# Performance work log

Measured on AMD Instinct MI355X. Metric: run time of the kernel, lower is better.

The kernel has to match this reference:

```python
import jax, jax.numpy as jnp
import numpy as np

HID = 256
N, D, K, EPOCHS = 100000, 512, 5, 2


def _lin(x, w, b):
    return x @ w.T + b


def setup_inputs() -> dict:
    key = jax.random.key(0)
    ks = jax.random.split(key, 16)
    s = 0.05
    return {
        "x0": jax.random.normal(ks[0], (N, D), jnp.float32),
        "x1": jax.random.normal(ks[1], (N, D), jnp.float32),
        "Hin0_w": jax.random.normal(ks[2], (HID, D), jnp.float32) * s,
        "Hin0_b": jax.random.normal(ks[3], (HID,), jnp.float32) * s,
        "Hin1_w": jax.random.normal(ks[4], (HID, D), jnp.float32) * s,
        "Hin1_b": jax.random.normal(ks[5], (HID,), jnp.float32) * s,
        "w0_w": jax.random.normal(ks[6], (HID, HID), jnp.float32) * s,
        "w0_b": jax.random.normal(ks[7], (HID,), jnp.float32) * s,
        "w1_w": jax.random.normal(ks[8], (HID, HID), jnp.float32) * s,
        "w1_b": jax.random.normal(ks[9], (HID,), jnp.float32) * s,
        "w2_w": jax.random.normal(ks[10], (HID, HID), jnp.float32) * s,
        "w2_b": jax.random.normal(ks[11], (HID,), jnp.float32) * s,
        "edge0": jax.random.randint(ks[12], (2, N * K), 0, N, dtype=jnp.int32),
        "edge1": jax.random.randint(ks[13], (2, N * K), 0, N, dtype=jnp.int32),
        "k": K,
        "update_epoch": EPOCHS,
    }


def reference(x0, x1, Hin0_w, Hin0_b, Hin1_w, Hin1_b, w0_w, w0_b,
              w1_w, w1_b, w2_w, w2_b, edge0, edge1, k, update_epoch):
    xs = (x0, x1)
    edges = (edge0, edge1)
    Hws = ((Hin0_w, Hin0_b), (Hin1_w, Hin1_b))
    n_views = len(xs)

    # per-view input projections: h_init[v] = H_ins[v](train_view[v])
    h_inits = [_lin(x, w, b) for x, (w, b) in zip(xs, Hws)]

    finals = []
    for v in range(n_views):
        # neighbor table: node i's k neighbors are edge[1][i*k : (i+1)*k]
        nbr_idx = edges[v][1].reshape(-1, k)  # [N, k]
        # cross-view self term: mean over other views of w2(h_init_other)
        slf = _lin(h_inits[1 - v], w2_w, w2_b)  # [N, HID] (nv-1 == 1)
        h = h_inits[v]
        for _ in range(update_epoch):
            h = _lin(h, w0_w, w0_b)
            # mean_j w1(h[nbr_j]) == w1(mean_j h[nbr_j]) since w1 is affine
            nbr_mean = h[nbr_idx].mean(axis=1)  # [N, HID] gather + reduce
            h = h + _lin(nbr_mean, w1_w, w1_b) + slf
        finals.append(jax.nn.relu(h))

    # average final embeddings across views
    h_out = sum(finals) / n_views
    return h_out
```

## Files before the change

kernel.cpp:

```cpp
#include <hip/hip_runtime.h>

#define NN 100000
#define DD 512
#define HH 256
#define KNB 5

typedef __attribute__((ext_vector_type(8))) short short8v;
typedef __attribute__((ext_vector_type(4))) short short4v;
typedef __attribute__((ext_vector_type(4))) float float4v;

static __device__ __forceinline__ float bf2f(unsigned short u) {
  union { unsigned int i; float f; } c;
  c.i = ((unsigned int)u) << 16;
  return c.f;
}
static __device__ __forceinline__ unsigned short f2bf(float f) {
  union { float f; unsigned int i; } c;
  c.f = f;
  unsigned int u = c.i;
  u += 0x7FFFu + ((u >> 16) & 1u);
  return (unsigned short)(u >> 16);
}

#define GLOAD16(g, l) __builtin_amdgcn_global_load_lds( \
    (const __attribute__((address_space(1))) unsigned int*)(g), \
    (__attribute__((address_space(3))) unsigned int*)(l), 16, 0, 0)

__global__ void cvt2(const float* __restrict__ s0, short* __restrict__ d0,
                     const float* __restrict__ s1, short* __restrict__ d1) {
  const int S1 = (HH * DD) / 4;
  int i = blockIdx.x * blockDim.x + threadIdx.x;
  if (i >= 2 * S1) return;
  const float* s = (i < S1) ? s0 : s1;
  short* d = (i < S1) ? d0 : d1;
  int j = (i < S1) ? i : i - S1;
  float4 v = reinterpret_cast<const float4*>(s)[j];
  short4v o;
  o[0] = (short)f2bf(v.x); o[1] = (short)f2bf(v.y);
  o[2] = (short)f2bf(v.z); o[3] = (short)f2bf(v.w);
  reinterpret_cast<short4v*>(d)[j] = o;
}

__global__ void prep_w01(const float* __restrict__ w0, const float* __restrict__ w1,
                         const float* __restrict__ w2, const float* __restrict__ b0,
                         const float* __restrict__ b1, const float* __restrict__ b2,
                         short* __restrict__ Bcat, float* __restrict__ bc) {
  int i = blockIdx.x;
  int j = threadIdx.x;
  Bcat[(size_t)i * 768 + j]       = (short)f2bf(w0[i * 256 + j]);
  Bcat[(size_t)i * 768 + 512 + j] = (short)f2bf(w2[i * 256 + j]);
  float acc = 0.f;
  for (int k = 0; k < 256; ++k)
    acc = fmaf(w1[i * 256 + k], w0[k * 256 + j], acc);
  Bcat[(size_t)i * 768 + 256 + j] = (short)f2bf(acc);
  if (j == 0) {
    float s = b0[i] + b1[i] + b2[i];
    for (int k = 0; k < 256; ++k) s = fmaf(w1[i * 256 + k], b0[k], s);
    bc[i] = s;
  }
}

__global__ __launch_bounds__(512) void proj_k(
    const float* __restrict__ Af0, const float* __restrict__ Af1,
    const short* __restrict__ Bw0, const short* __restrict__ Bw1,
    const float* __restrict__ bi0, const float* __restrict__ bi1,
    short* __restrict__ Cb0, short* __restrict__ Cb1)
{
  const float* Af = blockIdx.y ? Af1 : Af0;
  const short* Bw = blockIdx.y ? Bw1 : Bw0;
  const float* bias = blockIdx.y ? bi1 : bi0;
  short* Cb = blockIdx.y ? Cb1 : Cb0;

  __shared__ __align__(16) char BsRaw[256 * 64 * 2];
  __shared__ __align__(16) char AsRaw[128 * 64 * 4];

  const int tid = threadIdx.x;
  const int lane = tid & 63;
  const int wave = tid >> 6;
  const int wr = wave >> 2;
  const int wc = wave & 3;
  const int row0 = blockIdx.x * 128;

  float4v acc[4][4];
#pragma unroll
  for (int m = 0; m < 4; ++m)
#pragma unroll
    for (int n = 0; n < 4; ++n) acc[m][n] = (float4v)0.f;

  for (int k0 = 0; k0 < DD; k0 += 64) {
#pragma unroll
    for (int q = 0; q < 4; ++q) {
      int ch = q * 512 + tid;
      int r = ch >> 3, pc = ch & 7;
      int lc = pc ^ (r & 7);
      GLOAD16(Bw + (size_t)r * DD + k0 + lc * 8, BsRaw + (q * 512 + wave * 64) * 16);
    }
#pragma unroll
    for (int q = 0; q < 4; ++q) {
      int ch = q * 512 + tid;
      int r = ch >> 4, pc = ch & 15;
      int lc = pc ^ (r & 15);
      int rg = min(row0 + r, NN - 1);
      GLOAD16(Af + (size_t)rg * DD + k0 + lc * 4, AsRaw + (q * 512 + wave * 64) * 16);
    }
    __syncthreads();

#pragma unroll
    for (int kk = 0; kk < 2; ++kk) {
      const int ckb = kk * 4 + (lane >> 4);
      short8v a[4], b[4];
#pragma unroll
      for (int n = 0; n < 4; ++n) {
        int rb = wc * 64 + n * 16 + (lane & 15);
        b[n] = *reinterpret_cast<const short8v*>(BsRaw + rb * 128 + ((ckb ^ (rb & 7)) << 4));
      }
#pragma unroll
      for (int m = 0; m < 4; ++m) {
        int ra = wr * 64 + m * 16 + (lane & 15);
        int ck0 = kk * 8 + (lane >> 4) * 2;
        float4v f0 = *reinterpret_cast<const float4v*>(AsRaw + ra * 256 + ((ck0 ^ (ra & 15)) << 4));
        float4v f1 = *reinterpret_cast<const float4v*>(AsRaw + ra * 256 + (((ck0 + 1) ^ (ra & 15)) << 4));
        short8v av;
        av[0] = (short)f2bf(f0[0]); av[1] = (short)f2bf(f0[1]);
        av[2] = (short)f2bf(f0[2]); av[3] = (short)f2bf(f0[3]);
        av[4] = (short)f2bf(f1[0]); av[5] = (short)f2bf(f1[1]);
        av[6] = (short)f2bf(f1[2]); av[7] = (short)f2bf(f1[3]);
        a[m] = av;
      }
#pragma unroll
      for (int m = 0; m < 4; ++m)
#pragma unroll
        for (int n = 0; n < 4; ++n)
          acc[m][n] = __builtin_amdgcn_mfma_f32_16x16x32_bf16(b[n], a[m], acc[m][n], 0, 0, 0);
    }
    __syncthreads();
  }

  const int crow = lane & 15;
  const int cg = (lane >> 4) * 4;
#pragma unroll
  for (int m = 0; m < 4; ++m) {
    int rg = row0 + wr * 64 + m * 16 + crow;
    if (rg >= NN) continue;
#pragma unroll
    for (int n = 0; n < 4; ++n) {
      int colb = wc * 64 + n * 16 + cg;
      size_t off = (size_t)rg * HH + colb;
      float4v bi = *reinterpret_cast<const float4v*>(bias + colb);
      short4v o;
#pragma unroll
      for (int i = 0; i < 4; ++i) o[i] = (short)f2bf(acc[m][n][i] + bi[i]);
      *reinterpret_cast<short4v*>(Cb + off) = o;
    }
  }
}

template<int EPI>
__global__ __launch_bounds__(512) void epoch2(
    const short* __restrict__ D0_, const short* __restrict__ C0_,
    short* __restrict__ O0_, const int* __restrict__ n0_,
    const short* __restrict__ D1_, const short* __restrict__ C1_,
    short* __restrict__ O1_, const int* __restrict__ n1_,
    const short* __restrict__ Bw, const float* __restrict__ bias,
    float* __restrict__ Of, const short* __restrict__ Fin)
{
  __shared__ __align__(16) char BsRaw[2 * 16384];
  __shared__ __align__(16) char AsRaw[2 * 8192];
  __shared__ int nbrL[128][KNB];

  const short* D  = blockIdx.y ? D1_ : D0_;
  const short* Cc = blockIdx.y ? C1_ : C0_;
  short* Ob       = blockIdx.y ? O1_ : O0_;
  const int* nbr  = blockIdx.y ? n1_ : n0_;

  const int tid = threadIdx.x;
  const int lane = tid & 63;
  const int wave = tid >> 6;
  const int wr = wave >> 2;
  const int wc = wave & 3;
  const int row0 = blockIdx.x * 128;

  for (int e = tid; e < 128 * KNB; e += 512) {
    int r = e / KNB;
    int rg = min(row0 + r, NN - 1);
    nbrL[r][e - r * KNB] = nbr[rg * KNB + (e - r * KNB)];
  }

  {
#pragma unroll
    for (int q = 0; q < 2; ++q) {
      int ch = q * 512 + tid;
      int r = ch >> 2, pc = ch & 3;
      int lc = pc ^ ((r >> 1) & 3);
      GLOAD16(Bw + (size_t)r * 768 + lc * 8, BsRaw + (q * 512 + wave * 64) * 16);
    }
    int r = tid >> 2, pc = tid & 3;
    int lc = pc ^ ((r >> 1) & 3);
    int rg = min(row0 + r, NN - 1);
    GLOAD16(D + (size_t)rg * HH + lc * 8, AsRaw + (wave * 64) * 16);
  }
  __syncthreads();

  float4v acc[4][4];
#pragma unroll
  for (int m = 0; m < 4; ++m)
#pragma unroll
    for (int n = 0; n < 4; ++n) acc[m][n] = (float4v)0.f;

  for (int s = 0; s < 24; ++s) {
    const int sn = s + 1;
    if (sn < 24) {
      char* Bn = BsRaw + (sn & 1) * 16384;
#pragma unroll
      for (int q = 0; q < 2; ++q) {
        int ch = q * 512 + tid;
        int r = ch >> 2, pc = ch & 3;
        int lc = pc ^ ((r >> 1) & 3);
        GLOAD16(Bw + (size_t)r * 768 + sn * 32 + lc * 8, Bn + (q * 512 + wave * 64) * 16);
      }
      char* An = AsRaw + (sn & 1) * 8192;
      int r = tid >> 2, pc = tid & 3;
      int lc = pc ^ ((r >> 1) & 3);
      if (sn < 8 || sn >= 16) {
        const short* Ps = (sn < 8) ? (D + sn * 32) : (Cc + (sn * 32 - 512));
        int rg = min(row0 + r, NN - 1);
        GLOAD16(Ps + (size_t)rg * HH + lc * 8, An + (wave * 64) * 16);
      } else {
        const int kb = sn * 32 - 256;
        const short* Dk = D + kb + lc * 8;
        float a8[8] = {0.f, 0.f, 0.f, 0.f, 0.f, 0.f, 0.f, 0.f};
#pragma unroll
        for (int j = 0; j < KNB; ++j) {
          short8v v = *reinterpret_cast<const short8v*>(Dk + (size_t)nbrL[r][j] * HH);
#pragma unroll
          for (int x = 0; x < 8; ++x) a8[x] += bf2f((unsigned short)v[x]);
        }
        short8v o;
#pragma unroll
        for (int x = 0; x < 8; ++x) o[x] = (short)f2bf(a8[x] * 0.2f);
        *reinterpret_cast<short8v*>(An + tid * 16) = o;
      }
    }
    {
      const char* Bc = BsRaw + (s & 1) * 16384;
      const char* Ac = AsRaw + (s & 1) * 8192;
      const int ckb = lane >> 4;
      short8v a[4], b[4];
#pragma unroll
      for (int n = 0; n < 4; ++n) {
        int rb = wc * 64 + n * 16 + (lane & 15);
        b[n] = *reinterpret_cast<const short8v*>(Bc + rb * 64 + ((ckb ^ ((rb >> 1) & 3)) << 4));
      }
#pragma unroll
      for (int m = 0; m < 4; ++m) {
        int ra = wr * 64 + m * 16 + (lane & 15);
        a[m] = *reinterpret_cast<const short8v*>(Ac + ra * 64 + ((ckb ^ ((ra >> 1) & 3)) << 4));
      }
#pragma unroll
      for (int m = 0; m < 4; ++m)
#pragma unroll
        for (int n = 0; n < 4; ++n)
          acc[m][n] = __builtin_amdgcn_mfma_f32_16x16x32_bf16(b[n], a[m], acc[m][n], 0, 0, 0);
    }
    __syncthreads();
  }

  const int crow = lane & 15;
  const int cg = (lane >> 4) * 4;
#pragma unroll
  for (int m = 0; m < 4; ++m) {
    int rg = row0 + wr * 64 + m * 16 + crow;
    if (rg >= NN) continue;
#pragma unroll
    for (int n = 0; n < 4; ++n) {
      int colb = wc * 64 + n * 16 + cg;
      size_t off = (size_t)rg * HH + colb;
      float4v bi = *reinterpret_cast<const float4v*>(bias + colb);
      float v[4];
#pragma unroll
      for (int i = 0; i < 4; ++i) v[i] = acc[m][n][i] + bi[i];
      if constexpr (EPI >= 2) {
#pragma unroll
        for (int i = 0; i < 4; ++i) v[i] = fmaxf(v[i], 0.f);
      }
      if constexpr (EPI <= 2) {
        short4v o;
#pragma unroll
        for (int i = 0; i < 4; ++i) o[i] = (short)f2bf(v[i]);
        *reinterpret_cast<short4v*>(Ob + off) = o;
      } else {
        short4v f4 = *reinterpret_cast<const short4v*>(Fin + off);
        float4v o;
#pragma unroll
        for (int i = 0; i < 4; ++i)
          o[i] = (v[i] + bf2f((unsigned short)f4[i])) * 0.5f;
        *reinterpret_cast<float4v*>(Of + off) = o;
      }
    }
  }
}

extern "C" void kernel_launch(void* const* d_in, const int* in_sizes, int n_in,
                              void* d_out, int out_size, void* d_ws, size_t ws_size,
                              hipStream_t stream) {
  const float* x0  = (const float*)d_in[0];
  const float* x1  = (const float*)d_in[1];
  const float* wh0 = (const float*)d_in[2];
  const float* bh0 = (const float*)d_in[3];
  const float* wh1 = (const float*)d_in[4];
  const float* bh1 = (const float*)d_in[5];
  const float* w0  = (const float*)d_in[6];
  const float* b0  = (const float*)d_in[7];
  const float* w1  = (const float*)d_in[8];
  const float* b1  = (const float*)d_in[9];
  const float* w2  = (const float*)d_in[10];
  const float* b2  = (const float*)d_in[11];
  const int* e0    = (const int*)d_in[12];
  const int* e1    = (const int*)d_in[13];
  const int* nbr0  = e0 + (size_t)NN * KNB;
  const int* nbr1  = e1 + (size_t)NN * KNB;
  float* out       = (float*)d_out;

  char* ws = (char*)d_ws;
  size_t off = 0;
  auto alloc = [&](size_t bytes) -> void* {
    off = (off + 255) & ~(size_t)255;
    void* p = ws + off;
    off += bytes;
    return p;
  };

  short* Wh0  = (short*)alloc((size_t)HH * DD * 2);
  short* Wh1  = (short*)alloc((size_t)HH * DD * 2);
  short* Bcat = (short*)alloc((size_t)HH * 768 * 2);
  float* bc   = (float*)alloc((size_t)HH * 4);
  const size_t NB = (size_t)NN * HH * 2;
  short* hi0 = (short*)alloc(NB);
  short* hi1 = (short*)alloc(NB);
  short* hb0 = (short*)alloc(NB);
  short* hb1 = (short*)alloc(NB);
  short* f0  = (short*)alloc(NB);

  cvt2<<<dim3(256), dim3(256), 0, stream>>>(wh0, Wh0, wh1, Wh1);
  prep_w01<<<dim3(256), dim3(256), 0, stream>>>(w0, w1, w2, b0, b1, b2, Bcat, bc);

  proj_k<<<dim3((NN + 127) / 128, 2), dim3(512), 0, stream>>>(
      x0, x1, Wh0, Wh1, bh0, bh1, hi0, hi1);

  dim3 ge((NN + 127) / 128);

  epoch2<0><<<dim3(ge.x, 2), dim3(512), 0, stream>>>(
      hi0, hi1, hb0, nbr0,  hi1, hi0, hb1, nbr1,  Bcat, bc, nullptr, nullptr);

  epoch2<2><<<dim3(ge.x, 1), dim3(512), 0, stream>>>(
      hb0, hi1, f0, nbr0,   hb0, hi1, f0, nbr0,   Bcat, bc, nullptr, nullptr);

  epoch2<3><<<dim3(ge.x, 1), dim3(512), 0, stream>>>(
      hb1, hi0, nullptr, nbr1,  hb1, hi0, nullptr, nbr1,  Bcat, bc, out, f0);

  (void)in_sizes; (void)n_in; (void)out_size; (void)ws_size;
}
```

Baseline: 630.1 us.

## Shrink projection tile, restructure epoch kernel to single-buffered K64 steps, split launches

The projection kernel now uses 64-row tiles with half the accumulators and A staging, and its launch bounds request more resident blocks. The epoch kernel drops the double-buffered K32 software pipeline for a single-buffered K64 loop with a sync after each load stage. The fused two-view launch is split into separate per-view launches. The aim is higher occupancy and less register and LDS pressure, with other resident blocks hiding latency. The cost is losing the explicit load/compute overlap inside each block and paying extra launches.

```diff
diff --git a/kernel.cpp b/kernel.cpp
--- a/kernel.cpp
+++ b/kernel.cpp
@@ -60,7 +60,7 @@
   }
 }
 
-__global__ __launch_bounds__(512) void proj_k(
+__global__ __launch_bounds__(512, 6) void proj_k(
     const float* __restrict__ Af0, const float* __restrict__ Af1,
     const short* __restrict__ Bw0, const short* __restrict__ Bw1,
     const float* __restrict__ bi0, const float* __restrict__ bi1,
@@ -72,18 +72,18 @@
   short* Cb = blockIdx.y ? Cb1 : Cb0;
 
   __shared__ __align__(16) char BsRaw[256 * 64 * 2];
-  __shared__ __align__(16) char AsRaw[128 * 64 * 4];
+  __shared__ __align__(16) char AsRaw[64 * 64 * 4];
 
   const int tid = threadIdx.x;
   const int lane = tid & 63;
   const int wave = tid >> 6;
   const int wr = wave >> 2;
   const int wc = wave & 3;
-  const int row0 = blockIdx.x * 128;
-
-  float4v acc[4][4];
-#pragma unroll
-  for (int m = 0; m < 4; ++m)
+  const int row0 = blockIdx.x * 64;
+
+  float4v acc[2][4];
+#pragma unroll
+  for (int m = 0; m < 2; ++m)
 #pragma unroll
     for (int n = 0; n < 4; ++n) acc[m][n] = (float4v)0.f;
 
@@ -96,7 +96,7 @@
       GLOAD16(Bw + (size_t)r * DD + k0 + lc * 8, BsRaw + (q * 512 + wave * 64) * 16);
     }
 #pragma unroll
-    for (int q = 0; q < 4; ++q) {
+    for (int q = 0; q < 2; ++q) {
       int ch = q * 512 + tid;
       int r = ch >> 4, pc = ch & 15;
       int lc = pc ^ (r & 15);
@@ -108,15 +108,15 @@
 #pragma unroll
     for (int kk = 0; kk < 2; ++kk) {
       const int ckb = kk * 4 + (lane >> 4);
-      short8v a[4], b[4];
+      short8v a[2], b[4];
 #pragma unroll
       for (int n = 0; n < 4; ++n) {
         int rb = wc * 64 + n * 16 + (lane & 15);
         b[n] = *reinterpret_cast<const short8v*>(BsRaw + rb * 128 + ((ckb ^ (rb & 7)) << 4));
       }
 #pragma unroll
-      for (int m = 0; m < 4; ++m) {
-        int ra = wr * 64 + m * 16 + (lane & 15);
+      for (int m = 0; m < 2; ++m) {
+        int ra = wr * 32 + m * 16 + (lane & 15);
         int ck0 = kk * 8 + (lane >> 4) * 2;
         float4v f0 = *reinterpret_cast<const float4v*>(AsRaw + ra * 256 + ((ck0 ^ (ra & 15)) << 4));
         float4v f1 = *reinterpret_cast<const float4v*>(AsRaw + ra * 256 + (((ck0 + 1) ^ (ra & 15)) << 4));
@@ -128,7 +128,7 @@
         a[m] = av;
       }
 #pragma unroll
-      for (int m = 0; m < 4; ++m)
+      for (int m = 0; m < 2; ++m)
 #pragma unroll
         for (int n = 0; n < 4; ++n)
           acc[m][n] = __builtin_amdgcn_mfma_f32_16x16x32_bf16(b[n], a[m], acc[m][n], 0, 0, 0);
@@ -139,8 +139,8 @@
   const int crow = lane & 15;
   const int cg = (lane >> 4) * 4;
 #pragma unroll
-  for (int m = 0; m < 4; ++m) {
-    int rg = row0 + wr * 64 + m * 16 + crow;
+  for (int m = 0; m < 2; ++m) {
+    int rg = row0 + wr * 32 + m * 16 + crow;
     if (rg >= NN) continue;
 #pragma unroll
     for (int n = 0; n < 4; ++n) {
@@ -156,22 +156,15 @@
 }
 
 template<int EPI>
-__global__ __launch_bounds__(512) void epoch2(
-    const short* __restrict__ D0_, const short* __restrict__ C0_,
-    short* __restrict__ O0_, const int* __restrict__ n0_,
-    const short* __restrict__ D1_, const short* __restrict__ C1_,
-    short* __restrict__ O1_, const int* __restrict__ n1_,
+__global__ __launch_bounds__(512, 4) void epoch_k(
+    const short* __restrict__ D, const short* __restrict__ Cc,
     const short* __restrict__ Bw, const float* __restrict__ bias,
-    float* __restrict__ Of, const short* __restrict__ Fin)
+    short* __restrict__ Ob, float* __restrict__ Of,
+    const short* __restrict__ Fin, const int* __restrict__ nbr)
 {
-  __shared__ __align__(16) char BsRaw[2 * 16384];
-  __shared__ __align__(16) char AsRaw[2 * 8192];
+  __shared__ __align__(16) char BsRaw[256 * 64 * 2];
+  __shared__ __align__(16) char AsRaw[128 * 64 * 2];
   __shared__ int nbrL[128][KNB];
-
-  const short* D  = blockIdx.y ? D1_ : D0_;
-  const short* Cc = blockIdx.y ? C1_ : C0_;
-  short* Ob       = blockIdx.y ? O1_ : O0_;
-  const int* nbr  = blockIdx.y ? n1_ : n0_;
 
   const int tid = threadIdx.x;
   const int lane = tid & 63;
@@ -186,75 +179,66 @@
     nbrL[r][e - r * KNB] = nbr[rg * KNB + (e - r * KNB)];
   }
 
-  {
-#pragma unroll
-    for (int q = 0; q < 2; ++q) {
+  float4v acc[4][4];
+#pragma unroll
+  for (int m = 0; m < 4; ++m)
+#pragma unroll
+    for (int n = 0; n < 4; ++n) acc[m][n] = (float4v)0.f;
+
+  for (int k0 = 0; k0 < 768; k0 += 64) {
+#pragma unroll
+    for (int q = 0; q < 4; ++q) {
       int ch = q * 512 + tid;
-      int r = ch >> 2, pc = ch & 3;
-      int lc = pc ^ ((r >> 1) & 3);
-      GLOAD16(Bw + (size_t)r * 768 + lc * 8, BsRaw + (q * 512 + wave * 64) * 16);
-    }
-    int r = tid >> 2, pc = tid & 3;
-    int lc = pc ^ ((r >> 1) & 3);
-    int rg = min(row0 + r, NN - 1);
-    GLOAD16(D + (size_t)rg * HH + lc * 8, AsRaw + (wave * 64) * 16);
-  }
-  __syncthreads();
-
-  float4v acc[4][4];
-#pragma unroll
-  for (int m = 0; m < 4; ++m)
-#pragma unroll
-    for (int n = 0; n < 4; ++n) acc[m][n] = (float4v)0.f;
-
-  for (int s = 0; s < 24; ++s) {
-    const int sn = s + 1;
-    if (sn < 24) {
-      char* Bn = BsRaw + (sn & 1) * 16384;
+      int r = ch >> 3, pc = ch & 7;
+      int lc = pc ^ (r & 7);
+      GLOAD16(Bw + (size_t)r * 768 + k0 + lc * 8, BsRaw + (q * 512 + wave * 64) * 16);
+    }
+    if (k0 < 256 || k0 >= 512) {
+      const short* H = (k0 < 256) ? (D + k0) : (Cc + (k0 - 512));
 #pragma unroll
       for (int q = 0; q < 2; ++q) {
         int ch = q * 512 + tid;
-        int r = ch >> 2, pc = ch & 3;
-        int lc = pc ^ ((r >> 1) & 3);
-        GLOAD16(Bw + (size_t)r * 768 + sn * 32 + lc * 8, Bn + (q * 512 + wave * 64) * 16);
-      }
-      char* An = AsRaw + (sn & 1) * 8192;
-      int r = tid >> 2, pc = tid & 3;
-      int lc = pc ^ ((r >> 1) & 3);
-      if (sn < 8 || sn >= 16) {
-        const short* Ps = (sn < 8) ? (D + sn * 32) : (Cc + (sn * 32 - 512));
+        int r = ch >> 3, pc = ch & 7;
+        int lc = pc ^ (r & 7);
         int rg = min(row0 + r, NN - 1);
-        GLOAD16(Ps + (size_t)rg * HH + lc * 8, An + (wave * 64) * 16);
-      } else {
-        const int kb = sn * 32 - 256;
-        const short* Dk = D + kb + lc * 8;
+        GLOAD16(H + (size_t)rg * HH + lc * 8, AsRaw + (q * 512 + wave * 64) * 16);
+      }
+    } else {
+      const int kb = k0 - 256;
+#pragma unroll
+      for (int q = 0; q < 2; ++q) {
+        int ch = q * 512 + tid;
+        int r = ch >> 3, pc = ch & 7;
+        int lc = pc ^ (r & 7);
         float a8[8] = {0.f, 0.f, 0.f, 0.f, 0.f, 0.f, 0.f, 0.f};
 #pragma unroll
         for (int j = 0; j < KNB; ++j) {
-          short8v v = *reinterpret_cast<const short8v*>(Dk + (size_t)nbrL[r][j] * HH);
+          int id = nbrL[r][j];
+          short8v v = *reinterpret_cast<const short8v*>(D + (size_t)id * HH + kb + lc * 8);
 #pragma unroll
           for (int x = 0; x < 8; ++x) a8[x] += bf2f((unsigned short)v[x]);
         }
         short8v o;
 #pragma unroll
         for (int x = 0; x < 8; ++x) o[x] = (short)f2bf(a8[x] * 0.2f);
-        *reinterpret_cast<short8v*>(An + tid * 16) = o;
-      }
-    }
-    {
-      const char* Bc = BsRaw + (s & 1) * 16384;
-      const char* Ac = AsRaw + (s & 1) * 8192;
-      const int ckb = lane >> 4;
+        *reinterpret_cast<short8v*>(AsRaw + ch * 16) = o;
+      }
+    }
+    __syncthreads();
+
+#pragma unroll
+    for (int kk = 0; kk < 2; ++kk) {
+      const int ckb = kk * 4 + (lane >> 4);
       short8v a[4], b[4];
 #pragma unroll
       for (int n = 0; n < 4; ++n) {
         int rb = wc * 64 + n * 16 + (lane & 15);
-        b[n] = *reinterpret_cast<const short8v*>(Bc + rb * 64 + ((ckb ^ ((rb >> 1) & 3)) << 4));
+        b[n] = *reinterpret_cast<const short8v*>(BsRaw + rb * 128 + ((ckb ^ (rb & 7)) << 4));
       }
 #pragma unroll
       for (int m = 0; m < 4; ++m) {
         int ra = wr * 64 + m * 16 + (lane & 15);
-        a[m] = *reinterpret_cast<const short8v*>(Ac + ra * 64 + ((ckb ^ ((ra >> 1) & 3)) << 4));
+        a[m] = *reinterpret_cast<const short8v*>(AsRaw + ra * 128 + ((ckb ^ (ra & 7)) << 4));
       }
 #pragma unroll
       for (int m = 0; m < 4; ++m)
@@ -344,19 +328,16 @@
   cvt2<<<dim3(256), dim3(256), 0, stream>>>(wh0, Wh0, wh1, Wh1);
   prep_w01<<<dim3(256), dim3(256), 0, stream>>>(w0, w1, w2, b0, b1, b2, Bcat, bc);
 
-  proj_k<<<dim3((NN + 127) / 128, 2), dim3(512), 0, stream>>>(
+  proj_k<<<dim3((NN + 63) / 64, 2), dim3(512), 0, stream>>>(
       x0, x1, Wh0, Wh1, bh0, bh1, hi0, hi1);
 
   dim3 ge((NN + 127) / 128);
 
-  epoch2<0><<<dim3(ge.x, 2), dim3(512), 0, stream>>>(
-      hi0, hi1, hb0, nbr0,  hi1, hi0, hb1, nbr1,  Bcat, bc, nullptr, nullptr);
-
-  epoch2<2><<<dim3(ge.x, 1), dim3(512), 0, stream>>>(
-      hb0, hi1, f0, nbr0,   hb0, hi1, f0, nbr0,   Bcat, bc, nullptr, nullptr);
-
-  epoch2<3><<<dim3(ge.x, 1), dim3(512), 0, stream>>>(
-      hb1, hi0, nullptr, nbr1,  hb1, hi0, nullptr, nbr1,  Bcat, bc, out, f0);
+  epoch_k<0><<<ge, dim3(512), 0, stream>>>(hi0, hi1, Bcat, bc, hb0, nullptr, nullptr, nbr0);
+  epoch_k<0><<<ge, dim3(512), 0, stream>>>(hi1, hi0, Bcat, bc, hb1, nullptr, nullptr, nbr1);
+
+  epoch_k<2><<<ge, dim3(512), 0, stream>>>(hb0, hi1, Bcat, bc, f0, nullptr, nullptr, nbr0);
+  epoch_k<3><<<ge, dim3(512), 0, stream>>>(hb1, hi0, Bcat, bc, nullptr, out, f0, nbr1);
 
   (void)in_sizes; (void)n_in; (void)out_size; (void)ws_size;
 }
```

Measured after the change: 539.5 us. -14.4%, faster.
